# Performance work log

Hardware: AMD Instinct MI355X
Metric: run time of the kernel (lower is better)

Reference implementation:

```python
import jax, jax.numpy as jnp
import numpy as np

K = 16          # knn neighbors (init kwarg k)
GROUPS = 4      # GroupNorm groups
EPS = 1e-5
SLOPE = 0.2     # LeakyReLU negative slope


def fps(xyz, n):
    """Farthest point sampling. xyz: (B,N,3) -> idx (B,n). First index is 0 (pointnet2 convention)."""
    B, N, _ = xyz.shape

    def step(carry, _):
        dist, last = carry
        p = jnp.take_along_axis(xyz, last[:, None, None], axis=1)  # (B,1,3)
        d = jnp.sum((xyz - p) ** 2, axis=-1)                       # (B,N)
        dist = jnp.minimum(dist, d)
        nxt = jnp.argmax(dist, axis=-1).astype(jnp.int32)
        return (dist, nxt), nxt

    init = (jnp.full((B, N), jnp.inf, xyz.dtype), jnp.zeros((B,), jnp.int32))
    _, idxs = jax.lax.scan(step, init, None, length=n - 1)  # (n-1, B)
    return jnp.concatenate([jnp.zeros((B, 1), jnp.int32), idxs.T], axis=1)


def graph_feature(cq, fq, ck, fk):
    """DGCNN edge features. cq:(B,Q,3) fq:(B,Q,C) ck:(B,N,3) fk:(B,N,C) -> (B,Q,K,2C)."""
    d2 = (jnp.sum(cq * cq, -1)[:, :, None]
          - 2.0 * jnp.einsum('bqc,bnc->bqn', cq, ck)
          + jnp.sum(ck * ck, -1)[:, None, :])        # (B,Q,N)
    _, idx = jax.lax.top_k(-d2, K)                    # (B,Q,K) nearest first
    nb = jax.vmap(lambda f_, i_: f_[i_])(fk, idx)     # (B,Q,K,C)
    ctr = jnp.broadcast_to(fq[:, :, None, :], nb.shape)
    return jnp.concatenate([nb - ctr, ctr], axis=-1)


def conv_gn_lrelu(y, W, gw, gb):
    """1x1 Conv2d (no bias) + GroupNorm(4) + LeakyReLU(0.2). y: (B,Q,K,Cin), W: (Cout,Cin)."""
    y = jnp.einsum('bqkc,oc->bqko', y, W)
    B, Q, Kk, C = y.shape
    yg = y.reshape(B, Q * Kk, GROUPS, C // GROUPS)
    m = yg.mean(axis=(1, 3), keepdims=True)
    v = yg.var(axis=(1, 3), keepdims=True)
    y = ((yg - m) * jax.lax.rsqrt(v + EPS)).reshape(B, Q, Kk, C) * gw + gb
    return jnp.where(y > 0, y, SLOPE * y)


def setup_inputs() -> dict:
    key = jax.random.key(0)
    ks = jax.random.split(key, 16)
    B, N = 8, 4096
    s = lambda k_, shape, scale=0.1: (jax.random.normal(k_, shape, jnp.float32) * scale)
    return {
        'x': jax.random.normal(ks[0], (B, N, 7), jnp.float32),
        'W_in': s(ks[1], (8, 3), 0.5), 'b_in': s(ks[2], (8,), 0.02),
        'W1': s(ks[3], (32, 16), 0.2), 'g1w': jnp.ones((32,), jnp.float32), 'g1b': jnp.zeros((32,), jnp.float32),
        'W2': s(ks[4], (64, 64), 0.1), 'g2w': jnp.ones((64,), jnp.float32), 'g2b': jnp.zeros((64,), jnp.float32),
        'W3': s(ks[5], (64, 128), 0.1), 'g3w': jnp.ones((64,), jnp.float32), 'g3b': jnp.zeros((64,), jnp.float32),
        'W4': s(ks[6], (128, 128), 0.1), 'g4w': jnp.ones((128,), jnp.float32), 'g4b': jnp.zeros((128,), jnp.float32),
        'num0': 1024,
    }


def reference(x, W_in, b_in, W1, g1w, g1b, W2, g2w, g2b, W3, g3w, g3b, W4, g4w, g4b, num0):
    coor, normal, plane = x[..., :3], x[..., 3:6], x[..., 6:7]   # (B,N,3),(B,N,3),(B,N,1)

    # input_trans: Conv1d(3,8,1)
    f = jnp.einsum('bnc,oc->bno', coor, W_in) + b_in             # (B,N,8)

    g = graph_feature(coor, f, coor, f)                          # (B,N,K,16)
    f = conv_gn_lrelu(g, W1, g1w, g1b).max(axis=2)               # (B,N,32)

    idx = fps(coor, num0)
    gather = lambda a: jnp.take_along_axis(a, idx[:, :, None], axis=1)
    coor_q, normal_q, plane_q, f_q = gather(coor), gather(normal), gather(plane), gather(f)

    g = graph_feature(coor_q, f_q, coor, f)                      # (B,num0,K,64)
    f = conv_gn_lrelu(g, W2, g2w, g2b).max(axis=2)               # (B,num0,64)
    coor, normal, plane = coor_q, normal_q, plane_q

    g = graph_feature(coor, f, coor, f)                          # (B,num0,K,128)
    f = conv_gn_lrelu(g, W3, g3w, g3b).max(axis=2)               # (B,num0,64)

    idx = fps(coor, num0)  # source uses num[0] again
    gather = lambda a: jnp.take_along_axis(a, idx[:, :, None], axis=1)
    coor_q, normal_q, plane_q, f_q = gather(coor), gather(normal), gather(plane), gather(f)

    g = graph_feature(coor_q, f_q, coor, f)                      # (B,num0,K,128)
    f = conv_gn_lrelu(g, W4, g4w, g4b).max(axis=2)               # (B,num0,128)

    return coor_q, f, normal_q, plane_q
```

## Files before the change

kernel.cpp:

```cpp
#include <hip/hip_runtime.h>
#include <cstdint>

static constexpr int B   = 8;
static constexpr int N0  = 4096;
static constexpr int NQ  = 1024;
static constexpr int KNB = 16;

__device__ __forceinline__ float wave_min_bcast_f32(float x) {
#define STEP_(ctrl)                                                                     \
  {                                                                                     \
    int t_ = __builtin_amdgcn_update_dpp(__float_as_int(x), __float_as_int(x), ctrl,    \
                                         0xf, 0xf, false);                              \
    x = fminf(x, __int_as_float(t_));                                                   \
  }
  STEP_(0x111) STEP_(0x112) STEP_(0x114) STEP_(0x118) STEP_(0x142) STEP_(0x143)
#undef STEP_
  return __int_as_float(__builtin_amdgcn_readlane(__float_as_int(x), 63));
}

__device__ __forceinline__ unsigned wave_min_bcast_u32(unsigned x) {
#define STEP_(ctrl)                                                                     \
  {                                                                                     \
    unsigned t_ = (unsigned)__builtin_amdgcn_update_dpp((int)x, (int)x, ctrl,           \
                                                        0xf, 0xf, false);               \
    x = (t_ < x) ? t_ : x;                                                              \
  }
  STEP_(0x111) STEP_(0x112) STEP_(0x114) STEP_(0x118) STEP_(0x142) STEP_(0x143)
#undef STEP_
  return (unsigned)__builtin_amdgcn_readlane((int)x, 63);
}

__device__ __forceinline__ unsigned long long wave_max_u64_l63(unsigned long long k) {
#define STEPU_(ctrl)                                                                    \
  {                                                                                     \
    unsigned lo_ = (unsigned)k, hi_ = (unsigned)(k >> 32);                              \
    unsigned plo_ = (unsigned)__builtin_amdgcn_update_dpp((int)lo_, (int)lo_, ctrl,     \
                                                          0xf, 0xf, false);             \
    unsigned phi_ = (unsigned)__builtin_amdgcn_update_dpp((int)hi_, (int)hi_, ctrl,     \
                                                          0xf, 0xf, false);             \
    unsigned long long pk_ = ((unsigned long long)phi_ << 32) | plo_;                   \
    if (pk_ > k) k = pk_;                                                               \
  }
  STEPU_(0x111) STEPU_(0x112) STEPU_(0x114) STEPU_(0x118) STEPU_(0x142) STEPU_(0x143)
#undef STEPU_
  return k;
}

__global__ void prep_kernel(const float* __restrict__ x,
                            const float* __restrict__ W_in,
                            const float* __restrict__ b_in,
                            float4* __restrict__ c4, float* __restrict__ nrm,
                            float* __restrict__ pl, float* __restrict__ f0) {
  int i = blockIdx.x * 256 + threadIdx.x;
  if (i >= B * N0) return;
  const float* xp = x + (size_t)i * 7;
  float cx = xp[0], cy = xp[1], cz = xp[2];
  float kk = __fadd_rn(__fadd_rn(__fmul_rn(cx, cx), __fmul_rn(cy, cy)), __fmul_rn(cz, cz));
  c4[i] = make_float4(cx, cy, cz, kk);
  nrm[i * 3 + 0] = xp[3]; nrm[i * 3 + 1] = xp[4]; nrm[i * 3 + 2] = xp[5];
  pl[i] = xp[6];
#pragma unroll
  for (int o = 0; o < 8; o++) {
    f0[(size_t)i * 8 + o] = cx * W_in[o * 3 + 0] + cy * W_in[o * 3 + 1] + cz * W_in[o * 3 + 2] + b_in[o];
  }
}

template <int M>
__device__ __forceinline__ void knn_body(int bq, int lane,
                                         const float4* __restrict__ q4,
                                         const float4* __restrict__ k4,
                                         int Q, int Nk, int* __restrict__ out) {
  int b = bq / Q;
  float4 q = q4[bq];
  const float4* kb = k4 + (size_t)b * Nk;
  float d[M];
#pragma unroll
  for (int i = 0; i < M; i++) {
    float4 kp = kb[i * 64 + lane];
    float dot = __fadd_rn(__fadd_rn(__fmul_rn(q.x, kp.x), __fmul_rn(q.y, kp.y)),
                          __fmul_rn(q.z, kp.z));
    d[i] = __fadd_rn(__fsub_rn(q.w, __fmul_rn(2.0f, dot)), kp.w);
  }
  unsigned long long mask = 0ull;
  float lv = 3.0e38f; int li = 0;
#pragma unroll
  for (int i = 0; i < M; i++) { if (d[i] < lv) { lv = d[i]; li = i; } }
  int mynb = 0;
  for (int r = 0; r < KNB; r++) {
    int n = li * 64 + lane;
    float wmin = wave_min_bcast_f32(lv);
    unsigned ci = (lv == wmin) ? (unsigned)n : 0xFFFFFFFFu;
    int wn = (int)wave_min_bcast_u32(ci);
    if (lane == r) mynb = wn;
    if (lane == (wn & 63)) {
      mask |= 1ull << (wn >> 6);
      lv = 3.0e38f; li = 0;
#pragma unroll
      for (int i = 0; i < M; i++) {
        bool dead = (mask >> i) & 1ull;
        float dv = dead ? 3.0e38f : d[i];
        if (dv < lv) { lv = dv; li = i; }
      }
    }
  }
  if (lane < KNB) out[(size_t)bq * KNB + lane] = mynb;
}

template <int CF, int CO>
__device__ __forceinline__ void ctry_body(int i, int total, const float* __restrict__ fq,
                                          const float* __restrict__ W,
                                          float* __restrict__ ctrY,
                                          const int* __restrict__ ridx, int Q, int Nsrc) {
  if (i >= total) return;
  int o = i % CO, bq = i / CO;
  const float* fp;
  if (ridx) {
    int b = bq / Q;
    fp = fq + ((size_t)b * Nsrc + ridx[bq]) * CF;
  } else {
    fp = fq + (size_t)bq * CF;
  }
  const float* wp = W + (size_t)o * (2 * CF) + CF;
  float acc = 0.f;
#pragma unroll
  for (int c = 0; c < CF; c++) acc = fmaf(fp[c], wp[c], acc);
  ctrY[i] = acc;
}

template <int NPTS>
__device__ __forceinline__ void fps_body(const float4* __restrict__ cb, int* w) {
  constexpr int BLK = 256;
  constexpr int M = NPTS / BLK;
  constexpr int NW = BLK / 64;
  __shared__ __align__(16) float2 sxy[NPTS];
  __shared__ float szz[NPTS];
  __shared__ __align__(16) unsigned long long skey[2][NW];
  const int tid = threadIdx.x;
  const int wid = tid >> 6, lane = tid & 63;
  float cx[M], cy[M], cz[M], dist[M];
#pragma unroll
  for (int i = 0; i < M; i++) {
    float4 p = cb[tid * M + i];
    cx[i] = p.x; cy[i] = p.y; cz[i] = p.z;
    dist[i] = 3.4e38f;
    sxy[tid * M + i] = make_float2(p.x, p.y);
    szz[tid * M + i] = p.z;
  }
  w[0] = w[1] = w[2] = w[3] = 0;
  float4 p0 = cb[0];
  float px = p0.x, py = p0.y, pz = p0.z;
  __syncthreads();
  for (int t = 1; t < NQ; t++) {
    float bv = -1.f; int bi = 0;
#pragma unroll
    for (int i = 0; i < M; i++) {
      float dx = __fsub_rn(cx[i], px), dy = __fsub_rn(cy[i], py), dz = __fsub_rn(cz[i], pz);
      float d = __fadd_rn(__fadd_rn(__fmul_rn(dx, dx), __fmul_rn(dy, dy)), __fmul_rn(dz, dz));
      float dd = dist[i]; dd = (d < dd) ? d : dd; dist[i] = dd;
      if (dd > bv) { bv = dd; bi = tid * M + i; }
    }
    unsigned long long k =
        ((unsigned long long)__float_as_uint(bv) << 12) | (unsigned)(4095 - bi);
    k = wave_max_u64_l63(k);
    int p = t & 1;
    if (lane == 63) skey[p][wid] = k;
    __syncthreads();
    ulonglong2 ab = *(const ulonglong2*)&skey[p][0];
    ulonglong2 cd = *(const ulonglong2*)&skey[p][2];
    unsigned long long m0 = (ab.x > ab.y) ? ab.x : ab.y;
    unsigned long long m1 = (cd.x > cd.y) ? cd.x : cd.y;
    unsigned long long mk = (m0 > m1) ? m0 : m1;
    int win = 4095 - (int)(mk & 0xFFFull);
    float2 pxy = sxy[win];
    px = pxy.x; py = pxy.y; pz = szz[win];
    if (t == tid) w[0] = win;
    if (t == tid + 256) w[1] = win;
    if (t == tid + 512) w[2] = win;
    if (t == tid + 768) w[3] = win;
  }
}

__global__ __launch_bounds__(256, 2) void mega1_kernel(
    const float4* __restrict__ c40, const float* __restrict__ nrm,
    const float* __restrict__ pl, const float* __restrict__ f0,
    const float* __restrict__ W1, int* __restrict__ idx1,
    float4* __restrict__ c4q1, float* __restrict__ nq1, float* __restrict__ pq1,
    int* __restrict__ knn1, float* __restrict__ ctrY1) {
  int blk = blockIdx.x;
  if (blk < 8) {
    const int b = blk, tid = threadIdx.x;
    const float4* cb = c40 + (size_t)b * N0;
    int w[4];
    fps_body<N0>(cb, w);
    int* idxb = idx1 + (size_t)b * NQ;
#pragma unroll
    for (int u = 0; u < 4; u++) {
      int r = tid + u * 256;
      int s = (u == 0 && tid == 0) ? 0 : w[u];
      idxb[r] = s;
      c4q1[(size_t)b * NQ + r] = cb[s];
      const float* np = nrm + ((size_t)b * N0 + s) * 3;
      float* ndp = nq1 + ((size_t)b * NQ + r) * 3;
      ndp[0] = np[0]; ndp[1] = np[1]; ndp[2] = np[2];
      pq1[(size_t)b * NQ + r] = pl[(size_t)b * N0 + s];
    }
  } else if (blk < 8 + 8192) {
    int bq = (blk - 8) * 4 + (threadIdx.x >> 6);
    knn_body<64>(bq, threadIdx.x & 63, c40, c40, N0, N0, knn1);
  } else {
    int i = (blk - (8 + 8192)) * 256 + threadIdx.x;
    ctry_body<8, 32>(i, B * N0 * 32, f0, W1, ctrY1, nullptr, 0, 0);
  }
}

__global__ __launch_bounds__(256, 2) void mega2_kernel(
    const float4* __restrict__ c40, const float4* __restrict__ c4q1,
    const float* __restrict__ nq1, const float* __restrict__ pq1,
    const float* __restrict__ f1, const int* __restrict__ idx1,
    const float* __restrict__ W2, int* __restrict__ idx2,
    float4* __restrict__ c4q2, float* __restrict__ cq2out,
    float* __restrict__ nq2out, float* __restrict__ pq2out,
    int* __restrict__ knn2, int* __restrict__ knn3, float* __restrict__ ctrY2) {
  int blk = blockIdx.x;
  if (blk < 8) {
    const int b = blk, tid = threadIdx.x;
    const float4* cqb = c4q1 + (size_t)b * NQ;
    int w[4];
    fps_body<NQ>(cqb, w);
    int* idxb = idx2 + (size_t)b * NQ;
#pragma unroll
    for (int u = 0; u < 4; u++) {
      int r = tid + u * 256;
      int s = (u == 0 && tid == 0) ? 0 : w[u];
      idxb[r] = s;
      float4 c = cqb[s];
      c4q2[(size_t)b * NQ + r] = c;
      float* cd = cq2out + ((size_t)b * NQ + r) * 3;
      cd[0] = c.x; cd[1] = c.y; cd[2] = c.z;
      const float* np = nq1 + ((size_t)b * NQ + s) * 3;
      float* ndp = nq2out + ((size_t)b * NQ + r) * 3;
      ndp[0] = np[0]; ndp[1] = np[1]; ndp[2] = np[2];
      pq2out[(size_t)b * NQ + r] = pq1[(size_t)b * NQ + s];
    }
  } else if (blk < 8 + 2048) {
    int bq = (blk - 8) * 4 + (threadIdx.x >> 6);
    knn_body<64>(bq, threadIdx.x & 63, c4q1, c40, NQ, N0, knn2);
  } else if (blk < 8 + 4096) {
    int bq = (blk - (8 + 2048)) * 4 + (threadIdx.x >> 6);
    knn_body<16>(bq, threadIdx.x & 63, c4q1, c4q1, NQ, NQ, knn3);
  } else {
    int i = (blk - (8 + 4096)) * 256 + threadIdx.x;
    ctry_body<32, 64>(i, B * NQ * 64, f1, W2, ctrY2, idx1, NQ, N0);
  }
}

__global__ __launch_bounds__(256, 4) void mega3_kernel(
    const float4* __restrict__ c4q1, const float4* __restrict__ c4q2,
    const float* __restrict__ f3, const int* __restrict__ idx2,
    const float* __restrict__ W4, int* __restrict__ knn4, float* __restrict__ ctrY4) {
  int blk = blockIdx.x;
  if (blk < 2048) {
    int bq = blk * 4 + (threadIdx.x >> 6);
    knn_body<16>(bq, threadIdx.x & 63, c4q2, c4q1, NQ, NQ, knn4);
  } else {
    int i = (blk - 2048) * 256 + threadIdx.x;
    ctry_body<64, 128>(i, B * NQ * 128, f3, W4, ctrY4, idx2, NQ, NQ);
  }
}

template <int CF, int CO>
__global__ void ctry_kernel(const float* __restrict__ fq, const float* __restrict__ W,
                            float* __restrict__ ctrY, int total) {
  int i = blockIdx.x * 256 + threadIdx.x;
  ctry_body<CF, CO>(i, total, fq, W, ctrY, nullptr, 0, 0);
}

template <int CF, int CO>
__global__ __launch_bounds__(256) void edgeconv_kernel(
    const float* __restrict__ fq, const float* __restrict__ fk,
    const int* __restrict__ knn, const float* __restrict__ Wfull,
    const float* __restrict__ ctrY, const int* __restrict__ ridx,
    float* __restrict__ ymin, float* __restrict__ ymax,
    float* __restrict__ gstats, int Q, int Nk) {
  constexpr int J = CO / 4;
  constexpr int SEC = J * CF + 8;
  __shared__ float Wl[4 * SEC];
  __shared__ float sstat[8];
  for (int t = threadIdx.x; t < CO * CF; t += 256) {
    int o = t / CF, c = t % CF;
    Wl[(o / J) * SEC + (o % J) * CF + c] = Wfull[(size_t)o * (2 * CF) + c];
  }
  if (threadIdx.x < 8) sstat[threadIdx.x] = 0.0f;
  __syncthreads();
  const int wid = threadIdx.x >> 6, lane = threadIdx.x & 63;
  const int bq = blockIdx.x * 4 + wid;
  const int b = bq / Q;
  const int g = lane >> 4, k = lane & 15;
  const int ni = knn[(size_t)bq * KNB + k];
  const float* nbp = fk + (size_t)(b * Nk + ni) * CF;
  const float* cp = ridx ? fq + ((size_t)b * Nk + ridx[bq]) * CF
                         : fq + (size_t)bq * CF;
  float acc[J];
#pragma unroll
  for (int j = 0; j < J; j++) acc[j] = 0.0f;
  const float* wg = &Wl[g * SEC];
#pragma unroll
  for (int c = 0; c < CF; c += 4) {
    float4 nb4 = *(const float4*)(nbp + c);
    float4 c4  = *(const float4*)(cp + c);
    float e0 = nb4.x - c4.x, e1 = nb4.y - c4.y, e2 = nb4.z - c4.z, e3 = nb4.w - c4.w;
#pragma unroll
    for (int j = 0; j < J; j++) {
      float4 w4 = *(const float4*)(wg + j * CF + c);
      acc[j] = fmaf(e0, w4.x, acc[j]);
      acc[j] = fmaf(e1, w4.y, acc[j]);
      acc[j] = fmaf(e2, w4.z, acc[j]);
      acc[j] = fmaf(e3, w4.w, acc[j]);
    }
  }
  float s = 0.f, s2 = 0.f;
  const float* cyp = ctrY + (size_t)bq * CO + g * J;
#pragma unroll
  for (int j = 0; j < J; j++) {
    float y = acc[j] + cyp[j];
    acc[j] = y;
    s += y; s2 = fmaf(y, y, s2);
  }
  float mn[J];
#pragma unroll
  for (int j = 0; j < J; j++) mn[j] = acc[j];
#pragma unroll
  for (int m = 1; m < 16; m <<= 1) {
#pragma unroll
    for (int j = 0; j < J; j++) {
      float a = __shfl_xor(acc[j], m); if (a > acc[j]) acc[j] = a;
      float c2 = __shfl_xor(mn[j], m); if (c2 < mn[j]) mn[j] = c2;
    }
    s  += __shfl_xor(s, m);
    s2 += __shfl_xor(s2, m);
  }
  if (k == 0) {
    float* mnp = ymin + (size_t)bq * CO + g * J;
    float* mxp = ymax + (size_t)bq * CO + g * J;
#pragma unroll
    for (int j = 0; j < J; j++) { mnp[j] = mn[j]; mxp[j] = acc[j]; }
    atomicAdd(&sstat[g], s);
    atomicAdd(&sstat[4 + g], s2);
  }
  __syncthreads();
  if (threadIdx.x < 8) atomicAdd(&gstats[b * 8 + threadIdx.x], sstat[threadIdx.x]);
}

template <int CO>
__global__ void gn_out_kernel(const float* __restrict__ ymin, const float* __restrict__ ymax,
                              const float* __restrict__ gstats, const float* __restrict__ gw,
                              const float* __restrict__ gb, float* __restrict__ fout,
                              int total, int Q, float inv_cnt) {
  int i = blockIdx.x * 256 + threadIdx.x;
  if (i >= total) return;
  constexpr int J = CO / 4;
  int o = i % CO; int bq = i / CO; int b = bq / Q;
  int g = o / J;
  float m  = gstats[b * 8 + g] * inv_cnt;
  float s2 = gstats[b * 8 + 4 + g] * inv_cnt;
  float rs = rsqrtf(s2 - m * m + 1e-5f);
  float sc = gw[o] * rs;
  float sel = (sc >= 0.f) ? ymax[i] : ymin[i];
  float v = (sel - m) * sc + gb[o];
  fout[i] = (v > 0.f) ? v : 0.2f * v;
}

extern "C" void kernel_launch(void* const* d_in, const int* in_sizes, int n_in,
                              void* d_out, int out_size, void* d_ws, size_t ws_size,
                              hipStream_t stream) {
  (void)in_sizes; (void)n_in; (void)out_size; (void)ws_size;
  const float* x    = (const float*)d_in[0];
  const float* W_in = (const float*)d_in[1];
  const float* b_in = (const float*)d_in[2];
  const float* W1   = (const float*)d_in[3];
  const float* g1w  = (const float*)d_in[4];
  const float* g1b  = (const float*)d_in[5];
  const float* W2   = (const float*)d_in[6];
  const float* g2w  = (const float*)d_in[7];
  const float* g2b  = (const float*)d_in[8];
  const float* W3   = (const float*)d_in[9];
  const float* g3w  = (const float*)d_in[10];
  const float* g3b  = (const float*)d_in[11];
  const float* W4   = (const float*)d_in[12];
  const float* g4w  = (const float*)d_in[13];
  const float* g4b  = (const float*)d_in[14];

  float* ws = (float*)d_ws;
  size_t o_c40  = 0;
  size_t o_nrm  = o_c40  + (size_t)B * N0 * 4;
  size_t o_pl   = o_nrm  + (size_t)B * N0 * 3;
  size_t o_f0   = o_pl   + (size_t)B * N0;
  size_t o_f1   = o_f0   + (size_t)B * N0 * 8;
  size_t o_ctrY = o_f1   + (size_t)B * N0 * 32;
  size_t o_ymin = o_ctrY + (size_t)B * N0 * 32;
  size_t o_ymax = o_ymin + (size_t)B * N0 * 32;
  size_t o_knnA = o_ymax + (size_t)B * N0 * 32;
  size_t o_knnB = o_knnA + (size_t)B * N0 * KNB;
  size_t o_gst  = o_knnB + (size_t)B * NQ * KNB;
  size_t o_idx1 = o_gst  + 4 * B * 8;
  size_t o_idx2 = o_idx1 + (size_t)B * NQ;
  size_t o_c4q1 = o_idx2 + (size_t)B * NQ;
  size_t o_c4q2 = o_c4q1 + (size_t)B * NQ * 4;
  size_t o_nq1  = o_c4q2 + (size_t)B * NQ * 4;
  size_t o_pq1  = o_nq1  + (size_t)B * NQ * 3;
  size_t o_f2   = o_pq1  + (size_t)B * NQ;
  size_t o_f3   = o_f2   + (size_t)B * NQ * 64;

  float4* c40  = (float4*)(ws + o_c40);
  float*  nrm  = ws + o_nrm;   float* pl   = ws + o_pl;
  float*  f0   = ws + o_f0;    float* f1   = ws + o_f1;
  float*  ctrY = ws + o_ctrY;  float* ymin = ws + o_ymin;  float* ymax = ws + o_ymax;
  int*    knnA = (int*)(ws + o_knnA);
  int*    knnB = (int*)(ws + o_knnB);
  float*  gst  = ws + o_gst;
  int*    idx1 = (int*)(ws + o_idx1);
  int*    idx2 = (int*)(ws + o_idx2);
  float4* c4q1 = (float4*)(ws + o_c4q1);
  float4* c4q2 = (float4*)(ws + o_c4q2);
  float*  nq1  = ws + o_nq1;   float* pq1  = ws + o_pq1;
  float*  f2   = ws + o_f2;    float* f3   = ws + o_f3;

  float* out  = (float*)d_out;
  float* cq2  = out;
  float* fout = out + (size_t)B * NQ * 3;
  float* nq2  = fout + (size_t)B * NQ * 128;
  float* pq2  = nq2 + (size_t)B * NQ * 3;

  hipMemsetAsync(gst, 0, 4 * B * 8 * sizeof(float), stream);

  prep_kernel<<<(B * N0 + 255) / 256, 256, 0, stream>>>(x, W_in, b_in, c40, nrm, pl, f0);

  mega1_kernel<<<8 + 8192 + 4096, 256, 0, stream>>>(c40, nrm, pl, f0, W1,
                                                    idx1, c4q1, nq1, pq1, knnA, ctrY);
  edgeconv_kernel<8, 32><<<B * N0 / 4, 256, 0, stream>>>(f0, f0, knnA, W1, ctrY, nullptr,
                                                         ymin, ymax, gst + 0, N0, N0);
  gn_out_kernel<32><<<(B * N0 * 32 + 255) / 256, 256, 0, stream>>>(
      ymin, ymax, gst + 0, g1w, g1b, f1, B * N0 * 32, N0, 1.0f / (4096.0f * 16.0f * 8.0f));

  mega2_kernel<<<8 + 2048 + 2048 + 2048, 256, 0, stream>>>(
      c40, c4q1, nq1, pq1, f1, idx1, W2, idx2, c4q2, cq2, nq2, pq2, knnA, knnB, ctrY);
  edgeconv_kernel<32, 64><<<B * NQ / 4, 256, 0, stream>>>(f1, f1, knnA, W2, ctrY, idx1,
                                                          ymin, ymax, gst + B * 8, NQ, N0);
  gn_out_kernel<64><<<(B * NQ * 64 + 255) / 256, 256, 0, stream>>>(
      ymin, ymax, gst + B * 8, g2w, g2b, f2, B * NQ * 64, NQ, 1.0f / (1024.0f * 16.0f * 16.0f));

  ctry_kernel<64, 64><<<(B * NQ * 64 + 255) / 256, 256, 0, stream>>>(f2, W3, ctrY, B * NQ * 64);
  edgeconv_kernel<64, 64><<<B * NQ / 4, 256, 0, stream>>>(f2, f2, knnB, W3, ctrY, nullptr,
                                                          ymin, ymax, gst + 2 * B * 8, NQ, NQ);
  gn_out_kernel<64><<<(B * NQ * 64 + 255) / 256, 256, 0, stream>>>(
      ymin, ymax, gst + 2 * B * 8, g3w, g3b, f3, B * NQ * 64, NQ, 1.0f / (1024.0f * 16.0f * 16.0f));

  mega3_kernel<<<2048 + 4096, 256, 0, stream>>>(c4q1, c4q2, f3, idx2, W4, knnB, ctrY);
  edgeconv_kernel<64, 128><<<B * NQ / 4, 256, 0, stream>>>(f3, f3, knnB, W4, ctrY, idx2,
                                                           ymin, ymax, gst + 3 * B * 8, NQ, NQ);
  gn_out_kernel<128><<<(B * NQ * 128 + 255) / 256, 256, 0, stream>>>(
      ymin, ymax, gst + 3 * B * 8, g4w, g4b, fout, B * NQ * 128, NQ, 1.0f / (1024.0f * 16.0f * 32.0f));
}
```

Measured before the change: 1.502 ms.

## Replace per-round wave argmin KNN with streaming sorted top-16 insertion

```diff
diff --git a/kernel.cpp b/kernel.cpp
--- a/kernel.cpp
+++ b/kernel.cpp
@@ -5,30 +5,6 @@
 static constexpr int N0  = 4096;
 static constexpr int NQ  = 1024;
 static constexpr int KNB = 16;
-
-__device__ __forceinline__ float wave_min_bcast_f32(float x) {
-#define STEP_(ctrl)                                                                     \
-  {                                                                                     \
-    int t_ = __builtin_amdgcn_update_dpp(__float_as_int(x), __float_as_int(x), ctrl,    \
-                                         0xf, 0xf, false);                              \
-    x = fminf(x, __int_as_float(t_));                                                   \
-  }
-  STEP_(0x111) STEP_(0x112) STEP_(0x114) STEP_(0x118) STEP_(0x142) STEP_(0x143)
-#undef STEP_
-  return __int_as_float(__builtin_amdgcn_readlane(__float_as_int(x), 63));
-}
-
-__device__ __forceinline__ unsigned wave_min_bcast_u32(unsigned x) {
-#define STEP_(ctrl)                                                                     \
-  {                                                                                     \
-    unsigned t_ = (unsigned)__builtin_amdgcn_update_dpp((int)x, (int)x, ctrl,           \
-                                                        0xf, 0xf, false);               \
-    x = (t_ < x) ? t_ : x;                                                              \
-  }
-  STEP_(0x111) STEP_(0x112) STEP_(0x114) STEP_(0x118) STEP_(0x142) STEP_(0x143)
-#undef STEP_
-  return (unsigned)__builtin_amdgcn_readlane((int)x, 63);
-}
 
 __device__ __forceinline__ unsigned long long wave_max_u64_l63(unsigned long long k) {
 #define STEPU_(ctrl)                                                                    \
@@ -65,45 +41,55 @@
   }
 }
 
-template <int M>
+template <int NC>
 __device__ __forceinline__ void knn_body(int bq, int lane,
                                          const float4* __restrict__ q4,
                                          const float4* __restrict__ k4,
                                          int Q, int Nk, int* __restrict__ out) {
   int b = bq / Q;
   float4 q = q4[bq];
-  const float4* kb = k4 + (size_t)b * Nk;
-  float d[M];
-#pragma unroll
-  for (int i = 0; i < M; i++) {
-    float4 kp = kb[i * 64 + lane];
-    float dot = __fadd_rn(__fadd_rn(__fmul_rn(q.x, kp.x), __fmul_rn(q.y, kp.y)),
-                          __fmul_rn(q.z, kp.z));
-    d[i] = __fadd_rn(__fsub_rn(q.w, __fmul_rn(2.0f, dot)), kp.w);
-  }
-  unsigned long long mask = 0ull;
-  float lv = 3.0e38f; int li = 0;
-#pragma unroll
-  for (int i = 0; i < M; i++) { if (d[i] < lv) { lv = d[i]; li = i; } }
-  int mynb = 0;
-  for (int r = 0; r < KNB; r++) {
-    int n = li * 64 + lane;
-    float wmin = wave_min_bcast_f32(lv);
-    unsigned ci = (lv == wmin) ? (unsigned)n : 0xFFFFFFFFu;
-    int wn = (int)wave_min_bcast_u32(ci);
-    if (lane == r) mynb = wn;
-    if (lane == (wn & 63)) {
-      mask |= 1ull << (wn >> 6);
-      lv = 3.0e38f; li = 0;
-#pragma unroll
-      for (int i = 0; i < M; i++) {
-        bool dead = (mask >> i) & 1ull;
-        float dv = dead ? 3.0e38f : d[i];
-        if (dv < lv) { lv = dv; li = i; }
+  const float4* kb = k4 + (size_t)b * Nk + lane;
+  const float INF    = __int_as_float(0x7f800000);
+  const float NEGINF = __int_as_float(0xff800000);
+  float myd = INF;
+  int   myi = 0;
+  float kth = INF;
+  const bool isl0 = (lane & 15) == 0;
+  constexpr int G = (NC >= 8) ? 8 : NC;
+  for (int c0 = 0; c0 < NC; c0 += G) {
+    float dg[G];
+#pragma unroll
+    for (int u = 0; u < G; u++) {
+      float4 kp = kb[(c0 + u) * 64];
+      float dot = __fadd_rn(__fadd_rn(__fmul_rn(q.x, kp.x), __fmul_rn(q.y, kp.y)),
+                            __fmul_rn(q.z, kp.z));
+      dg[u] = __fadd_rn(__fsub_rn(q.w, __fmul_rn(2.0f, dot)), kp.w);
+    }
+#pragma unroll
+    for (int u = 0; u < G; u++) {
+      float d = dg[u];
+      unsigned long long m = __ballot(d < kth);
+      while (m) {
+        int j = __builtin_ctzll(m);
+        float dv = __int_as_float(__builtin_amdgcn_readlane(__float_as_int(d), j));
+        int   iv = (c0 + u) * 64 + j;
+        bool gt = (myd > dv);
+        float pd = __int_as_float(__builtin_amdgcn_update_dpp(
+            0, __float_as_int(myd), 0x111, 0xf, 0xf, true));
+        int   pi = __builtin_amdgcn_update_dpp(0, myi, 0x111, 0xf, 0xf, true);
+        pd = isl0 ? NEGINF : pd;
+        bool tp = (pd > dv);
+        float nd = tp ? pd : dv;
+        int   ni = tp ? pi : iv;
+        myd = gt ? nd : myd;
+        myi = gt ? ni : myi;
+        kth = __int_as_float(__builtin_amdgcn_readlane(__float_as_int(myd), 15));
+        m = __ballot(d < kth);
+        m = (j < 63) ? (m & (~0ull << (j + 1))) : 0ull;
       }
     }
   }
-  if (lane < KNB) out[(size_t)bq * KNB + lane] = mynb;
+  if (lane < KNB) out[(size_t)bq * KNB + lane] = myi;
 }
 
 template <int CF, int CO>
```

Result: no change. 1.508 ms (+0.4%).
